# Kernel optimization log

Measured on AMD Instinct MI355X. Metric: run time of the kernel, lower is better.

## Reference

```python
import jax, jax.numpy as jnp
import numpy as np
import math

B, T, D, H = 4, 2048, 2048, 16
HD = D // H  # 128


def rotate_half(x):
    half = x.shape[-1] // 2
    return jnp.concatenate([-x[..., half:], x[..., :half]], axis=-1)


def apply_rope(x, cos, sin):
    # x: [B,H,T,hd]; cos/sin: [T,hd] -> broadcast over B,H
    return x * cos[None, None] + rotate_half(x) * sin[None, None]


def setup_inputs() -> dict:
    key = jax.random.key(0)
    ks = jax.random.split(key, 6)
    x = jax.random.normal(ks[0], (B, T, D), dtype=jnp.float32)
    # standard RoPE tables
    inv_freq = 1.0 / (10000.0 ** (np.arange(0, HD, 2, dtype=np.float32) / HD))
    freqs = np.arange(T, dtype=np.float32)[:, None] * inv_freq[None, :]  # [T, hd/2]
    emb = np.concatenate([freqs, freqs], axis=-1)  # [T, hd]
    cos = jnp.asarray(np.cos(emb))
    sin = jnp.asarray(np.sin(emb))
    # additive causal mask [T,T]: 0 on/below diagonal, -1e9 above
    mask = jnp.where(jnp.tril(jnp.ones((T, T), dtype=bool)), 0.0, -1e9).astype(jnp.float32)
    scale = 0.02
    Wq = scale * jax.random.normal(ks[1], (D, D), dtype=jnp.float32)
    Wk = scale * jax.random.normal(ks[2], (D, D), dtype=jnp.float32)
    Wv = scale * jax.random.normal(ks[3], (D, D), dtype=jnp.float32)
    Wo = scale * jax.random.normal(ks[4], (D, D), dtype=jnp.float32)
    return {"x": x, "cos": cos, "sin": sin, "mask": mask,
            "Wq": Wq, "Wk": Wk, "Wv": Wv, "Wo": Wo}


def reference(x, cos, sin, mask, Wq, Wk, Wv, Wo):
    b, t, d = x.shape

    def split_heads(y):  # [B,T,D] -> [B,H,T,hd]
        return y.reshape(b, t, H, HD).transpose(0, 2, 1, 3)

    # nn.Linear: y = x @ W.T
    Q = apply_rope(split_heads(jnp.einsum('btd,od->bto', x, Wq)), cos, sin)
    K = apply_rope(split_heads(jnp.einsum('btd,od->bto', x, Wk)), cos, sin)
    V = split_heads(jnp.einsum('btd,od->bto', x, Wv))

    scores = jnp.einsum('bhqd,bhkd->bhqk', Q, K) / math.sqrt(HD)
    scores = scores + mask  # [T,T] broadcasts over [B,H,T,T]
    weights = jax.nn.softmax(scores, axis=-1)
    out = jnp.einsum('bhqk,bhkd->bhqd', weights, V)
    out = out.transpose(0, 2, 1, 3).reshape(b, t, d)
    return jnp.einsum('btd,od->bto', out, Wo)
```

## Files before the change

kernel.cpp:

```cpp
#include <hip/hip_runtime.h>
#include <hip/hip_bf16.h>

#define DEV static __device__ __forceinline__

typedef __attribute__((ext_vector_type(8))) _Float16 half8;
typedef __attribute__((ext_vector_type(4))) float f32x4;

constexpr int Bc = 4, Tc = 2048, Dc = 2048, Hc = 16;

DEV ushort f2h(float f) { _Float16 h = (_Float16)f; return __builtin_bit_cast(ushort, h); }
DEV float  h2f(ushort u) { return (float)__builtin_bit_cast(_Float16, u); }

DEV f32x4 MFMA(half8 a, half8 b, f32x4 c) {
  return __builtin_amdgcn_mfma_f32_16x16x32_f16(a, b, c, 0, 0, 0);
}

DEV void async_cp16(void* lds, const void* g) {
  __builtin_amdgcn_global_load_lds((const __attribute__((address_space(1))) void*)g,
                                   (__attribute__((address_space(3))) void*)lds,
                                   16, 0, 0);
}

__global__ __launch_bounds__(256) void cvt(const float* __restrict__ in,
                                           ushort* __restrict__ out, int n4) {
  const int i = blockIdx.x * 256 + threadIdx.x;
  if (i >= n4) return;
  const float4 v = ((const float4*)in)[i];
  ushort4 o;
  o.x = f2h(v.x); o.y = f2h(v.y); o.z = f2h(v.z); o.w = f2h(v.w);
  ((ushort4*)out)[i] = o;
}

template <typename OutT>
__global__ __launch_bounds__(512, 2) void gemm256(const ushort* __restrict__ A,
                                                  const ushort* __restrict__ Bw,
                                                  OutT* __restrict__ C) {
  __shared__ ushort As[3][256 * 32];
  __shared__ ushort Bs[3][256 * 32];
  const int tid = threadIdx.x;
  const int lane = tid & 63, wid = tid >> 6;
  const int g = lane >> 4, q16 = lane & 15;
  const int wm = wid >> 2, wn = wid & 3;

  const int flat = (int)blockIdx.x;
  const int xcd = flat & 7, idx = flat >> 3;
  const int bm = xcd * 4 + (idx & 3);
  const int bn = idx >> 2;
  const ushort* Ab = A + (size_t)bm * 256 * Dc;
  const ushort* Bb = Bw + (size_t)bn * 256 * Dc;

#define STAGE(P, K0, DST) do {                                                 \
    _Pragma("unroll") for (int p_ = 0; p_ < 2; ++p_) {                         \
      const int c_ = p_ * 512 + tid;                                           \
      const int row_ = c_ >> 2, gl_ = c_ & 3;                                  \
      async_cp16(&(DST)[(p_ * 512 + wid * 64) * 8],                            \
                 (P) + (size_t)row_ * Dc + (K0) +                              \
                 ((gl_ ^ ((row_ >> 1) & 3)) << 3));                            \
    }                                                                          \
  } while (0)

  f32x4 acc[8][4] = {};

  STAGE(Ab, 0, As[0]);  STAGE(Bb, 0, Bs[0]);
  STAGE(Ab, 32, As[1]); STAGE(Bb, 32, Bs[1]);
  STAGE(Ab, 64, As[2]); STAGE(Bb, 64, Bs[2]);
  asm volatile("s_waitcnt vmcnt(8)" ::: "memory");
  __builtin_amdgcn_s_barrier();
  __builtin_amdgcn_sched_barrier(0);

  const int sgz = (g ^ ((q16 >> 1) & 3)) << 3;

  int buf = 0;
#pragma unroll 1
  for (int t = 0; t < 64; ++t) {
    const ushort* Asb = As[buf];
    const ushort* Bsb = Bs[buf];
    half8 af[8], bf[4];
#pragma unroll
    for (int mf = 0; mf < 8; ++mf) {
      const int r = wm * 128 + mf * 16 + q16;
      af[mf] = *(const half8*)&Asb[r * 32 + sgz];
    }
#pragma unroll
    for (int nf = 0; nf < 4; ++nf) {
      const int r = wn * 64 + nf * 16 + q16;
      bf[nf] = *(const half8*)&Bsb[r * 32 + sgz];
    }
    __builtin_amdgcn_s_setprio(1);
#pragma unroll
    for (int mf = 0; mf < 8; ++mf)
#pragma unroll
      for (int nf = 0; nf < 4; ++nf)
        acc[mf][nf] = MFMA(af[mf], bf[nf], acc[mf][nf]);
    __builtin_amdgcn_s_setprio(0);

    __builtin_amdgcn_s_barrier();
    __builtin_amdgcn_sched_barrier(0);
    if (t + 3 < 64) {
      STAGE(Ab, (t + 3) * 32, As[buf]);
      STAGE(Bb, (t + 3) * 32, Bs[buf]);
    }
    if (t + 3 < 64)      asm volatile("s_waitcnt vmcnt(8)" ::: "memory");
    else if (t + 2 < 64) asm volatile("s_waitcnt vmcnt(4)" ::: "memory");
    else                 asm volatile("s_waitcnt vmcnt(0)" ::: "memory");
    __builtin_amdgcn_s_barrier();
    __builtin_amdgcn_sched_barrier(0);
    buf = (buf == 2) ? 0 : buf + 1;
  }
#undef STAGE

  const int m00 = bm * 256 + wm * 128 + g * 4;
  const int n0 = bn * 256 + wn * 64 + q16;
#pragma unroll
  for (int mf = 0; mf < 8; ++mf)
#pragma unroll
    for (int nf = 0; nf < 4; ++nf) {
      const int m0 = m00 + mf * 16;
      const int n = n0 + nf * 16;
#pragma unroll
      for (int r = 0; r < 4; ++r) {
        const float v = acc[mf][nf][r];
        if constexpr (sizeof(OutT) == 2)
          C[(size_t)(m0 + r) * Dc + n] = (OutT)f2h(v);
        else
          C[(size_t)(m0 + r) * Dc + n] = (OutT)v;
      }
    }
}

__global__ __launch_bounds__(256) void rope(ushort* __restrict__ X,
                                            const float* __restrict__ cs,
                                            const float* __restrict__ sn) {
  const int tid = blockIdx.x * 256 + threadIdx.x;
  const int row = tid >> 4;
  const int jq = (tid & 15) << 2;
  const int t = (row >> 4) & (Tc - 1);
  ushort* base = X + (size_t)row * 128;
  const ushort4 lo = *(const ushort4*)(base + jq);
  const ushort4 hi = *(const ushort4*)(base + 64 + jq);
  const float4 c4 = *(const float4*)(cs + t * 128 + jq);
  const float4 s4 = *(const float4*)(sn + t * 128 + jq);
  const float xl[4] = {h2f(lo.x), h2f(lo.y), h2f(lo.z), h2f(lo.w)};
  const float xh[4] = {h2f(hi.x), h2f(hi.y), h2f(hi.z), h2f(hi.w)};
  const float cc[4] = {c4.x, c4.y, c4.z, c4.w};
  const float ss[4] = {s4.x, s4.y, s4.z, s4.w};
  ushort4 olo, ohi;
  ushort* po = (ushort*)&olo;
  ushort* ph = (ushort*)&ohi;
#pragma unroll
  for (int k = 0; k < 4; ++k) {
    po[k] = f2h(xl[k] * cc[k] - xh[k] * ss[k]);
    ph[k] = f2h(xh[k] * cc[k] + xl[k] * ss[k]);
  }
  *(ushort4*)(base + jq) = olo;
  *(ushort4*)(base + 64 + jq) = ohi;
}

__global__ __launch_bounds__(512, 2) void attn(const ushort* __restrict__ Q,
                                               const ushort* __restrict__ K,
                                               const ushort* __restrict__ V,
                                               ushort* __restrict__ O) {
  __shared__ ushort Ks[2][64 * 128];
  __shared__ ushort Vt[2][128 * 64];

  const int tid = threadIdx.x;
  const int lane = tid & 63, wid = tid >> 6;
  const int g = lane >> 4, q16 = lane & 15;

  const int flat = (int)(blockIdx.x + 4 * blockIdx.y);
  const int xcd = flat & 7, idx = flat >> 3;
  const int bh = xcd + 8 * (idx & 7);
  const int pr = idx >> 3;

  const int b = bh >> 4, h = bh & 15;
  const size_t headbase = ((size_t)b * Tc * Hc + h) * 128;
  const float SCL2 = 0.12751743f;

  const int vdc = (wid & 3) * 4 + (lane & 3);
  const int vkvp = (wid >> 2) * 16 + (lane >> 2);

  uint4 vreg[2];

#define ISSUEK(KT, BUF) do {                                                   \
    const ushort* Kb_ = K + headbase + (size_t)(KT) * 64 * Dc;                 \
    _Pragma("unroll") for (int i_ = 0; i_ < 2; ++i_) {                         \
      const int c_ = i_ * 512 + tid;                                           \
      const int kv_ = c_ >> 4, gl_ = c_ & 15;                                  \
      async_cp16(&Ks[BUF][(i_ * 512 + wid * 64) * 8],                          \
                 Kb_ + (size_t)kv_ * Dc + ((gl_ ^ (kv_ & 7)) << 3));           \
    }                                                                          \
  } while (0)

#define LOADV(KT) do {                                                         \
    const ushort* p0_ = V + headbase + (size_t)((KT) * 64 + 2 * vkvp) * Dc +   \
                        vdc * 8;                                               \
    vreg[0] = *(const uint4*)p0_;                                              \
    vreg[1] = *(const uint4*)(p0_ + Dc);                                       \
  } while (0)

#define WRITEV(BUF) do {                                                       \
    const ushort* e0_ = (const ushort*)&vreg[0];                               \
    const ushort* e1_ = (const ushort*)&vreg[1];                               \
    _Pragma("unroll") for (int j_ = 0; j_ < 8; ++j_) {                         \
      const int d_ = vdc * 8 + j_;                                             \
      const unsigned w_ = (unsigned)e0_[j_] | ((unsigned)e1_[j_] << 16);       \
      *(unsigned*)&Vt[BUF][(d_ * 64 + 2 * vkvp) ^ ((d_ & 7) << 3)] = w_;       \
    }                                                                          \
  } while (0)

#pragma unroll 1
  for (int half = 0; half < 2; ++half) {
    const int q0 = (half ? pr : 7 - pr) * 256;
    const int qrow = q0 + wid * 32;
    const int nt = q0 / 64 + 4;

    half8 qreg[2][4];
#pragma unroll
    for (int qf = 0; qf < 2; ++qf)
#pragma unroll
      for (int ds = 0; ds < 4; ++ds)
        qreg[qf][ds] = *(const half8*)(Q + headbase +
                       (size_t)(qrow + qf * 16 + q16) * Dc + ds * 32 + g * 8);

    f32x4 oacc[2][8] = {};
    float m_[2] = {-1e30f, -1e30f};
    float l_[2] = {0.f, 0.f};

    __builtin_amdgcn_s_barrier();
    __builtin_amdgcn_sched_barrier(0);
    ISSUEK(0, 0);
    LOADV(0);
    WRITEV(0);

#pragma unroll 1
    for (int kt = 0; kt < nt; ++kt) {
      const int cur = kt & 1;
      const int kv0 = kt * 64;
      asm volatile("s_waitcnt vmcnt(0) lgkmcnt(0)" ::: "memory");
      __builtin_amdgcn_s_barrier();
      __builtin_amdgcn_sched_barrier(0);
      if (kt + 1 < nt) {
        ISSUEK(kt + 1, cur ^ 1);
        LOADV(kt + 1);
      }

      if (kv0 <= qrow + 31) {
        const ushort* Ksb = Ks[cur];
        const ushort* Vtb = Vt[cur];
        f32x4 s[2][4] = {};
        __builtin_amdgcn_s_setprio(1);
#pragma unroll
        for (int ds = 0; ds < 4; ++ds) {
          half8 kf[4];
#pragma unroll
          for (int kvf = 0; kvf < 4; ++kvf) {
            const int kv = kvf * 16 + q16;
            kf[kvf] = *(const half8*)&Ksb[(kv * 128 + ds * 32 + g * 8) ^ ((kv & 7) << 3)];
          }
#pragma unroll
          for (int kvf = 0; kvf < 4; ++kvf)
#pragma unroll
            for (int qf = 0; qf < 2; ++qf)
              s[qf][kvf] = MFMA(kf[kvf], qreg[qf][ds], s[qf][kvf]);
        }
        __builtin_amdgcn_s_setprio(0);
        float pmax[2] = {-1e30f, -1e30f};
        if (kv0 + 63 > qrow) {
#pragma unroll
          for (int qf = 0; qf < 2; ++qf) {
            const int qg = qrow + qf * 16 + q16;
#pragma unroll
            for (int kvf = 0; kvf < 4; ++kvf)
#pragma unroll
              for (int r = 0; r < 4; ++r) {
                float v = s[qf][kvf][r];
                if ((kv0 + kvf * 16 + g * 4 + r) > qg) v = -1e30f;
                s[qf][kvf][r] = v;
                pmax[qf] = fmaxf(pmax[qf], v);
              }
          }
        } else {
#pragma unroll
          for (int qf = 0; qf < 2; ++qf)
#pragma unroll
            for (int kvf = 0; kvf < 4; ++kvf)
#pragma unroll
              for (int r = 0; r < 4; ++r)
                pmax[qf] = fmaxf(pmax[qf], s[qf][kvf][r]);
        }
#pragma unroll
        for (int qf = 0; qf < 2; ++qf) {
          pmax[qf] = fmaxf(pmax[qf], __shfl_xor(pmax[qf], 16));
          pmax[qf] = fmaxf(pmax[qf], __shfl_xor(pmax[qf], 32));
        }
        if (!__all((pmax[0] <= m_[0] + 16.f) & (pmax[1] <= m_[1] + 16.f))) {
#pragma unroll
          for (int qf = 0; qf < 2; ++qf) {
            const float mn2 = fmaxf(m_[qf], pmax[qf]);
            const float alpha = __builtin_exp2f((m_[qf] - mn2) * SCL2);
            m_[qf] = mn2;
            l_[qf] *= alpha;
#pragma unroll
            for (int df = 0; df < 8; ++df)
              oacc[qf][df] *= alpha;
          }
        }
        uint w[2][4][2];
#pragma unroll
        for (int qf = 0; qf < 2; ++qf) {
          const float mn = m_[qf];
          float lsum = 0.f;
#pragma unroll
          for (int kvf = 0; kvf < 4; ++kvf) {
            const float p0 = __builtin_exp2f((s[qf][kvf][0] - mn) * SCL2);
            const float p1 = __builtin_exp2f((s[qf][kvf][1] - mn) * SCL2);
            const float p2 = __builtin_exp2f((s[qf][kvf][2] - mn) * SCL2);
            const float p3 = __builtin_exp2f((s[qf][kvf][3] - mn) * SCL2);
            lsum += (p0 + p1) + (p2 + p3);
            w[qf][kvf][0] = (unsigned)f2h(p0) | ((unsigned)f2h(p1) << 16);
            w[qf][kvf][1] = (unsigned)f2h(p2) | ((unsigned)f2h(p3) << 16);
          }
          l_[qf] += lsum;
        }
        const bool ghi = g >= 2;
        const bool godd = (g & 1) != 0;
        half8 pb[2][2];
#pragma unroll
        for (int qf = 0; qf < 2; ++qf) {
          uint sA[2][2], sB[2][2];
#pragma unroll
          for (int c = 0; c < 2; ++c)
#pragma unroll
            for (int i = 0; i < 2; ++i) {
              sA[c][i] = ghi ? w[qf][2 * c + 1][i] : w[qf][2 * c][i];
              sB[c][i] = ghi ? w[qf][2 * c][i] : w[qf][2 * c + 1][i];
            }
          uint x16[2][2], x32[2][2], x48[2][2];
#pragma unroll
          for (int c = 0; c < 2; ++c)
#pragma unroll
            for (int i = 0; i < 2; ++i) {
              x16[c][i] = __shfl_xor(sA[c][i], 16);
              x32[c][i] = __shfl_xor(sB[c][i], 32);
              x48[c][i] = __shfl_xor(sB[c][i], 48);
            }
#pragma unroll
          for (int c = 0; c < 2; ++c) {
            uint4 t;
            t.x = godd ? (ghi ? x16[c][0] : x48[c][0]) : (ghi ? x32[c][0] : sA[c][0]);
            t.y = godd ? (ghi ? x16[c][1] : x48[c][1]) : (ghi ? x32[c][1] : sA[c][1]);
            t.z = godd ? (ghi ? sA[c][0] : x32[c][0]) : (ghi ? x48[c][0] : x16[c][0]);
            t.w = godd ? (ghi ? sA[c][1] : x32[c][1]) : (ghi ? x48[c][1] : x16[c][1]);
            pb[qf][c] = __builtin_bit_cast(half8, t);
          }
        }
        __builtin_amdgcn_s_setprio(1);
#pragma unroll
        for (int c = 0; c < 2; ++c) {
#pragma unroll
          for (int df = 0; df < 8; ++df) {
            const int d = df * 16 + q16;
            const half8 vf = *(const half8*)&Vtb[(d * 64 + c * 32 + g * 8) ^ ((d & 7) << 3)];
#pragma unroll
            for (int qf = 0; qf < 2; ++qf)
              oacc[qf][df] = MFMA(vf, pb[qf][c], oacc[qf][df]);
          }
        }
        __builtin_amdgcn_s_setprio(0);
      }

      if (kt + 1 < nt) WRITEV(cur ^ 1);
    }

#pragma unroll
    for (int qf = 0; qf < 2; ++qf) {
      float l = l_[qf];
      l += __shfl_xor(l, 16);
      l += __shfl_xor(l, 32);
      const float inv = 1.0f / l;
      const int t = qrow + qf * 16 + q16;
#pragma unroll
      for (int df = 0; df < 8; ++df) {
        const f32x4 v = oacc[qf][df];
        ushort4 o;
        o.x = f2h(v[0] * inv); o.y = f2h(v[1] * inv);
        o.z = f2h(v[2] * inv); o.w = f2h(v[3] * inv);
        *(ushort4*)(O + headbase + (size_t)t * Dc + df * 16 + g * 4) = o;
      }
    }
  }
#undef ISSUEK
#undef LOADV
#undef WRITEV
}

extern "C" void kernel_launch(void* const* d_in, const int* in_sizes, int n_in,
                              void* d_out, int out_size, void* d_ws, size_t ws_size,
                              hipStream_t stream) {
  (void)in_sizes; (void)n_in; (void)out_size; (void)ws_size;
  const float* x  = (const float*)d_in[0];
  const float* cs = (const float*)d_in[1];
  const float* sn = (const float*)d_in[2];
  const float* Wq = (const float*)d_in[4];
  const float* Wk = (const float*)d_in[5];
  const float* Wv = (const float*)d_in[6];
  const float* Wo = (const float*)d_in[7];
  float* out = (float*)d_out;

  char* ws = (char*)d_ws;
  const size_t MB = 1024 * 1024;
  ushort* xb  = (ushort*)(ws);
  ushort* wqb = (ushort*)(ws + 32 * MB);
  ushort* wkb = (ushort*)(ws + 40 * MB);
  ushort* wvb = (ushort*)(ws + 48 * MB);
  ushort* wob = (ushort*)(ws + 56 * MB);
  ushort* Qr  = (ushort*)(ws + 64 * MB);
  ushort* Kr  = (ushort*)(ws + 96 * MB);
  ushort* Vr  = (ushort*)(ws + 128 * MB);

  cvt<<<16384, 256, 0, stream>>>(x, xb, 4194304);
  cvt<<<4096, 256, 0, stream>>>(Wq, wqb, 1048576);
  cvt<<<4096, 256, 0, stream>>>(Wk, wkb, 1048576);
  cvt<<<4096, 256, 0, stream>>>(Wv, wvb, 1048576);
  cvt<<<4096, 256, 0, stream>>>(Wo, wob, 1048576);

  gemm256<ushort><<<256, 512, 0, stream>>>(xb, wqb, Qr);
  gemm256<ushort><<<256, 512, 0, stream>>>(xb, wkb, Kr);
  gemm256<ushort><<<256, 512, 0, stream>>>(xb, wvb, Vr);

  rope<<<8192, 256, 0, stream>>>(Qr, cs, sn);
  rope<<<8192, 256, 0, stream>>>(Kr, cs, sn);

  attn<<<dim3(4, 64), 512, 0, stream>>>(Qr, Kr, Vr, xb);

  gemm256<float><<<256, 512, 0, stream>>>(xb, wob, out);
}
```

Baseline: 538.8 us.

## Split GEMM k-step into four phases interleaving async loads with MFMA

The 256x256 GEMM main loop moves to four LDS buffers. Each k-step is split into four quadrant phases, and each phase issues one async global-to-LDS copy, waits, barriers, then runs an 8-MFMA sub-block. This spreads memory traffic across the compute and drops the end-of-iteration barrier pair, aiming to overlap loads with MFMA more finely. In exchange it raises LDS use, adds more barriers per k-step, and uses a fixed vmcnt(8) wait that may be too loose in the tail iterations when no new loads are issued.

```diff
diff --git a/kernel.cpp b/kernel.cpp
--- a/kernel.cpp
+++ b/kernel.cpp
@@ -35,8 +35,8 @@
 __global__ __launch_bounds__(512, 2) void gemm256(const ushort* __restrict__ A,
                                                   const ushort* __restrict__ Bw,
                                                   OutT* __restrict__ C) {
-  __shared__ ushort As[3][256 * 32];
-  __shared__ ushort Bs[3][256 * 32];
+  __shared__ ushort As[4][256 * 32];
+  __shared__ ushort Bs[4][256 * 32];
   const int tid = threadIdx.x;
   const int lane = tid & 63, wid = tid >> 6;
   const int g = lane >> 4, q16 = lane & 15;
@@ -49,65 +49,71 @@
   const ushort* Ab = A + (size_t)bm * 256 * Dc;
   const ushort* Bb = Bw + (size_t)bn * 256 * Dc;
 
-#define STAGE(P, K0, DST) do {                                                 \
-    _Pragma("unroll") for (int p_ = 0; p_ < 2; ++p_) {                         \
-      const int c_ = p_ * 512 + tid;                                           \
-      const int row_ = c_ >> 2, gl_ = c_ & 3;                                  \
-      async_cp16(&(DST)[(p_ * 512 + wid * 64) * 8],                            \
-                 (P) + (size_t)row_ * Dc + (K0) +                              \
-                 ((gl_ ^ ((row_ >> 1) & 3)) << 3));                            \
-    }                                                                          \
+#define STAGE1(KT, BUF, PH) do {                                               \
+    const int pass_ = (PH) & 1;                                                \
+    const int c_ = pass_ * 512 + tid;                                          \
+    const int row_ = c_ >> 2, gl_ = c_ & 3;                                    \
+    const int col_ = (KT) * 32 + ((gl_ ^ ((row_ >> 1) & 3)) << 3);             \
+    if ((PH) < 2)                                                              \
+      async_cp16(&As[BUF][(pass_ * 512 + wid * 64) * 8],                       \
+                 Ab + (size_t)row_ * Dc + col_);                               \
+    else                                                                       \
+      async_cp16(&Bs[BUF][(pass_ * 512 + wid * 64) * 8],                       \
+                 Bb + (size_t)row_ * Dc + col_);                               \
   } while (0)
 
   f32x4 acc[8][4] = {};
 
-  STAGE(Ab, 0, As[0]);  STAGE(Bb, 0, Bs[0]);
-  STAGE(Ab, 32, As[1]); STAGE(Bb, 32, Bs[1]);
-  STAGE(Ab, 64, As[2]); STAGE(Bb, 64, Bs[2]);
-  asm volatile("s_waitcnt vmcnt(8)" ::: "memory");
+  for (int tt = 0; tt < 3; ++tt) {
+    STAGE1(tt, tt, 0); STAGE1(tt, tt, 1);
+    STAGE1(tt, tt, 2); STAGE1(tt, tt, 3);
+  }
+  asm volatile("s_waitcnt vmcnt(0)" ::: "memory");
   __builtin_amdgcn_s_barrier();
   __builtin_amdgcn_sched_barrier(0);
 
   const int sgz = (g ^ ((q16 >> 1) & 3)) << 3;
 
-  int buf = 0;
+#define PHASE(AA, BB, RDA, RDB, PH) do {                                       \
+    if (RDA) {                                                                 \
+      _Pragma("unroll") for (int mf_ = 0; mf_ < 4; ++mf_) {                    \
+        const int r_ = wm * 128 + (AA) * 64 + mf_ * 16 + q16;                  \
+        af[mf_] = *(const half8*)&Asb[r_ * 32 + sgz];                          \
+      }                                                                        \
+    }                                                                          \
+    if (RDB) {                                                                 \
+      _Pragma("unroll") for (int nf_ = 0; nf_ < 2; ++nf_) {                    \
+        const int r_ = wn * 64 + (BB) * 32 + nf_ * 16 + q16;                   \
+        bf[nf_] = *(const half8*)&Bsb[r_ * 32 + sgz];                          \
+      }                                                                        \
+    }                                                                          \
+    if (st) STAGE1(t + 3, sb, PH);                                             \
+    asm volatile("s_waitcnt vmcnt(8)" ::: "memory");                           \
+    __builtin_amdgcn_s_barrier();                                              \
+    __builtin_amdgcn_sched_barrier(0);                                         \
+    __builtin_amdgcn_s_setprio(1);                                             \
+    _Pragma("unroll") for (int mf_ = 0; mf_ < 4; ++mf_)                        \
+      _Pragma("unroll") for (int nf_ = 0; nf_ < 2; ++nf_)                      \
+        acc[(AA) * 4 + mf_][(BB) * 2 + nf_] =                                  \
+            MFMA(af[mf_], bf[nf_], acc[(AA) * 4 + mf_][(BB) * 2 + nf_]);       \
+    __builtin_amdgcn_s_setprio(0);                                             \
+  } while (0)
+
 #pragma unroll 1
   for (int t = 0; t < 64; ++t) {
-    const ushort* Asb = As[buf];
-    const ushort* Bsb = Bs[buf];
-    half8 af[8], bf[4];
-#pragma unroll
-    for (int mf = 0; mf < 8; ++mf) {
-      const int r = wm * 128 + mf * 16 + q16;
-      af[mf] = *(const half8*)&Asb[r * 32 + sgz];
-    }
-#pragma unroll
-    for (int nf = 0; nf < 4; ++nf) {
-      const int r = wn * 64 + nf * 16 + q16;
-      bf[nf] = *(const half8*)&Bsb[r * 32 + sgz];
-    }
-    __builtin_amdgcn_s_setprio(1);
-#pragma unroll
-    for (int mf = 0; mf < 8; ++mf)
-#pragma unroll
-      for (int nf = 0; nf < 4; ++nf)
-        acc[mf][nf] = MFMA(af[mf], bf[nf], acc[mf][nf]);
-    __builtin_amdgcn_s_setprio(0);
-
-    __builtin_amdgcn_s_barrier();
-    __builtin_amdgcn_sched_barrier(0);
-    if (t + 3 < 64) {
-      STAGE(Ab, (t + 3) * 32, As[buf]);
-      STAGE(Bb, (t + 3) * 32, Bs[buf]);
-    }
-    if (t + 3 < 64)      asm volatile("s_waitcnt vmcnt(8)" ::: "memory");
-    else if (t + 2 < 64) asm volatile("s_waitcnt vmcnt(4)" ::: "memory");
-    else                 asm volatile("s_waitcnt vmcnt(0)" ::: "memory");
-    __builtin_amdgcn_s_barrier();
-    __builtin_amdgcn_sched_barrier(0);
-    buf = (buf == 2) ? 0 : buf + 1;
+    const int rb = t & 3;
+    const int sb = (t + 3) & 3;
+    const bool st = (t + 3) < 64;
+    const ushort* Asb = As[rb];
+    const ushort* Bsb = Bs[rb];
+    half8 af[4], bf[2];
+    PHASE(0, 0, 1, 1, 0);
+    PHASE(0, 1, 0, 1, 1);
+    PHASE(1, 1, 1, 0, 2);
+    PHASE(1, 0, 0, 1, 3);
   }
-#undef STAGE
+#undef PHASE
+#undef STAGE1
 
   const int m00 = bm * 256 + wm * 128 + g * 4;
   const int n0 = bn * 256 + wn * 64 + q16;
```

Result: faster. 509.9 us (-5.4%).
